# Performance work log

Hardware: AMD Instinct MI355X
Metric: run time of the kernel (lower is better)

The kernel has to match this reference:

```python
import jax, jax.numpy as jnp
import numpy as np

S = 32
D = S * S          # d = 1024 grid points
DK = 64
R = 4              # heads
NB = 3             # blocks
IN_DIM = 64
EPS = 1e-5
DX = 2.0 / (S - 1)
DXDY = DX * DX
SCALE = 1.0 / np.sqrt(float(DK))


def _edge():
    # grid[i,j] = (gx[i], gx[j]); gridT is the transpose ordering
    gx = jnp.linspace(-1.0, 1.0, S, dtype=jnp.float32)
    g = jnp.stack(jnp.meshgrid(gx, gx, indexing='ij'), axis=-1)  # [S,S,2]
    grid = g.reshape(D, 2)
    gridT = g.transpose(1, 0, 2).reshape(D, 2)
    return jnp.concatenate([
        jnp.broadcast_to(grid[:, None, :], (D, D, 2)),
        jnp.broadcast_to(gridT[None, :, :], (D, D, 2)),
    ], axis=-1)  # [D, D, 4]


def _mlp(e, W1, b1, W2, b2, W3, b3):
    # DenseNet([4,32,64,1], LeakyReLU): two hidden LeakyReLU layers, linear head
    h = jax.nn.leaky_relu(e @ W1 + b1)
    h = jax.nn.leaky_relu(h @ W2 + b2)
    return h @ W3 + b3


def _ln(v, g, b):
    # LayerNorm over normalized_shape [2d, input_dim] -> reduce last two axes
    m = jnp.mean(v, axis=(1, 2), keepdims=True)
    var = jnp.var(v, axis=(1, 2), keepdims=True)
    return (v - m) * jax.lax.rsqrt(var + EPS) * g + b


def setup_inputs() -> dict:
    key = jax.random.key(0)
    ks = jax.random.split(key, 24)
    f32 = jnp.float32

    def nrm(k, shape, fan):
        return jax.random.normal(k, shape, f32) / np.sqrt(float(fan))

    inp = {
        'x': jax.random.normal(ks[0], (8, D, 1), f32),
        'xy': jax.random.normal(ks[1], (8, 2 * D, IN_DIM), f32),
        'P': jnp.zeros((1,), f32),
        # kernel MLP (edge -> weight)
        'kW1': nrm(ks[2], (4, 32), 4), 'kb1': jnp.zeros((32,), f32),
        'kW2': nrm(ks[3], (32, 64), 32), 'kb2': jnp.zeros((64,), f32),
        'kW3': nrm(ks[4], (64, 1), 64), 'kb3': jnp.zeros((1,), f32),
        # kernelf MLP (edge -> weightf)
        'fW1': nrm(ks[5], (4, 32), 4), 'fb1': jnp.zeros((32,), f32),
        'fW2': nrm(ks[6], (32, 64), 32), 'fb2': jnp.zeros((64,), f32),
        'fW3': nrm(ks[7], (64, 1), 64), 'fb3': jnp.zeros((1,), f32),
        # per-(block, head) Q/K linear layers
        'Wq': nrm(ks[8], (NB, R, IN_DIM, DK), IN_DIM),
        'bq': jnp.zeros((NB, R, DK), f32),
        'Wk': nrm(ks[9], (NB, R, IN_DIM, DK), IN_DIM),
        'bk': jnp.zeros((NB, R, DK), f32),
        # per-block LayerNorm affine params over [2d, input_dim]
        'ln_g': jnp.ones((NB, 2 * D, IN_DIM), f32),
        'ln_b': jnp.zeros((NB, 2 * D, IN_DIM), f32),
    }
    return inp


def _forward(x, xy, P, kW1, kb1, kW2, kb2, kW3, kb3,
             fW1, fb1, fW2, fb2, fW3, fb3, Wq, bq, Wk, bk, ln_g, ln_b):
    edge = _edge()
    weight = _mlp(edge, kW1, kb1, kW2, kb2, kW3, kb3).reshape(D, D)   # shared over batch
    weightf = _mlp(edge, fW1, fb1, fW2, fb2, fW3, fb3).reshape(D, D)

    Vinput = _ln(xy, ln_g[0], ln_b[0])  # [b, 2d, in]

    for j in range(NB - 1):
        mid = jnp.zeros_like(Vinput)
        for i in range(R):
            Q = Vinput @ Wq[j, i] + bq[j, i]  # [b, 2d, dk]
            K = Vinput @ Wk[j, i] + bk[j, i]
            Attn = jnp.einsum('bnk,bmk->bnm', Q, K) * SCALE  # [b, 2d, 2d]
            mid = mid + DXDY * jnp.einsum('bnm,bmi->bni', Attn, Vinput)
        Vinput = _ln(mid, ln_g[j + 1], ln_b[j + 1]) + Vinput

    b = xy.shape[0]
    out = jnp.zeros((b, IN_DIM, D), xy.dtype)
    xy_d = xy[:, :D, :]  # [b, d, in]
    for i in range(R):
        Q = Vinput @ Wq[NB - 1, i] + bq[NB - 1, i]
        K = Vinput @ Wk[NB - 1, i] + bk[NB - 1, i]
        Au = jnp.einsum('bnk,bmk->bnm', Q[:, :D], K[:, :D]) * SCALE  # Attn[:, :d, :d]
        Af = jnp.einsum('bnk,bmk->bnm', Q[:, D:], K[:, :D]) * SCALE  # Attn[:, d:, :d]
        Vu = DXDY * jnp.einsum('bnm,bmi->bin', Au, xy_d)  # [b, in, d]
        Vf = DXDY * jnp.einsum('bnm,bmi->bin', Af, xy_d)
        out = out + DXDY * (Vu @ weight) + DXDY * (Vf @ weightf)
    return out.transpose(0, 2, 1)  # [b, d, in]


def reference(x, xy, P, kW1, kb1, kW2, kb2, kW3, kb3,
              fW1, fb1, fW2, fb2, fW3, fb3, Wq, bq, Wk, bk, ln_g, ln_b):
    return _forward(x, xy, P, kW1, kb1, kW2, kb2, kW3, kb3,
                    fW1, fb1, fW2, fb2, fW3, fb3, Wq, bq, Wk, bk, ln_g, ln_b)
```

## Files before the change

kernel.cpp:

```cpp
#include <hip/hip_runtime.h>

namespace {
constexpr int SD = 1024;
constexpr int TD = 2048;
constexpr int BATCH = 8;
constexpr int RH = 4;
constexpr float EPSc = 1e-5f;
constexpr float DXf = 2.0f / 31.0f;
constexpr float DXDYf = DXf * DXf;
constexpr float SCALEf = 0.125f;
constexpr float CFINAL = DXDYf * DXDYf * SCALEf;

constexpr size_t OFF_V   = 0;
constexpr size_t OFF_MID = OFF_V   + (size_t)BATCH * TD * 64;
constexpr size_t OFF_W   = OFF_MID + (size_t)BATCH * TD * 64;
constexpr size_t OFF_WF  = OFF_W   + (size_t)SD * SD;
constexpr size_t OFF_U1K = OFF_WF  + (size_t)SD * SD;
constexpr size_t OFF_U2K = OFF_U1K + SD * 32;
constexpr size_t OFF_U1F = OFF_U2K + SD * 32;
constexpr size_t OFF_U2F = OFF_U1F + SD * 32;
constexpr size_t OFF_GP  = OFF_U2F + SD * 32;
constexpr size_t OFF_SP  = OFF_GP  + (size_t)BATCH * 32 * 4096;
constexpr size_t OFF_A   = OFF_SP  + BATCH * 32 * 64;
constexpr size_t OFF_RV  = OFF_A   + BATCH * 4096;
constexpr size_t OFF_LNP = OFF_RV  + BATCH * 64;
constexpr size_t OFF_ZU  = OFF_LNP + BATCH * 32 * 2;
constexpr size_t OFF_ZF  = OFF_ZU  + (size_t)SD * 512;
constexpr size_t OFF_W1  = OFF_ZF  + (size_t)SD * 512;
constexpr size_t OFF_CS  = OFF_W1  + SD;
constexpr size_t WS_FLOATS = OFF_CS + 16 * SD;
constexpr size_t LIN_OFF = 50704;
}

typedef __bf16 bf16x8 __attribute__((ext_vector_type(8)));
typedef float f32x4 __attribute__((ext_vector_type(4)));

__device__ __forceinline__ float leaky(float x) { return fmaxf(x, 0.01f * x); }
__device__ __forceinline__ float gxv(int i) { return -1.0f + (2.0f / 31.0f) * (float)i; }
__device__ __forceinline__ ushort f2bf(float x) { union { __bf16 b; ushort u; } v; v.b = (__bf16)x; return v.u; }
__device__ __forceinline__ float bf2f(ushort u) { return __uint_as_float(((uint)u) << 16); }

__global__ __launch_bounds__(256) void k_prep(
    const float* __restrict__ kW1, const float* __restrict__ kb1,
    const float* __restrict__ fW1, const float* __restrict__ fb1,
    float* __restrict__ u1k, float* __restrict__ u2k,
    float* __restrict__ u1f, float* __restrict__ u2f,
    const float* __restrict__ kW2, const float* __restrict__ kW3, const float* __restrict__ kb2,
    const float* __restrict__ fW2, const float* __restrict__ fW3, const float* __restrict__ fb2,
    float* __restrict__ LIN,
    const float* __restrict__ Wq, const float* __restrict__ bq,
    const float* __restrict__ Wk, const float* __restrict__ bk,
    float* __restrict__ Ep, float* __restrict__ fp,
    float* __restrict__ gp, float* __restrict__ cp,
    const float* __restrict__ xy, float* __restrict__ part) {
  __shared__ __align__(16) float Wqs[4096];
  __shared__ float Wks[64 * 65];
  __shared__ float bqs[64], bks[64];
  __shared__ float ss4[4], qq4[4];
  int blk = blockIdx.x, t = threadIdx.x;
  if (blk >= 16) {
    int idx = blk - 16;
    int b = idx >> 5, c = idx & 31;
    const float4* X4 = reinterpret_cast<const float4*>(xy + (size_t)b * 131072 + (size_t)c * 4096);
    float s = 0.f, q = 0.f;
#pragma unroll
    for (int k = 0; k < 4; k++) {
      float4 v = X4[t + k * 256];
      s += v.x + v.y + v.z + v.w;
      q += v.x * v.x + v.y * v.y + v.z * v.z + v.w * v.w;
    }
    for (int off = 32; off; off >>= 1) { s += __shfl_down(s, off); q += __shfl_down(q, off); }
    int lane = t & 63, wid = t >> 6;
    if (lane == 0) { ss4[wid] = s; qq4[wid] = q; }
    __syncthreads();
    if (t == 0) {
      part[(size_t)(b * 32 + c) * 2] = ss4[0] + ss4[1] + ss4[2] + ss4[3];
      part[(size_t)(b * 32 + c) * 2 + 1] = qq4[0] + qq4[1] + qq4[2] + qq4[3];
    }
    return;
  }
  if (blk < 4) {
    int n = blk * 256 + t;
    float ga = gxv(n >> 5), gb = gxv(n & 31);
    for (int j = 0; j < 32; j++) {
      u1k[n * 32 + j] = ga * kW1[j] + gb * kW1[32 + j] + kb1[j];
      u2k[n * 32 + j] = gb * kW1[64 + j] + ga * kW1[96 + j];
      u1f[n * 32 + j] = ga * fW1[j] + gb * fW1[32 + j] + fb1[j];
      u2f[n * 32 + j] = gb * fW1[64 + j] + ga * fW1[96 + j];
    }
    if (blk < 2 && t < 33) {
      const float* W2 = blk ? fW2 : kW2;
      const float* W3 = blk ? fW3 : kW3;
      const float* b2 = blk ? fb2 : kb2;
      if (t < 32) {
        float s = 0.f;
        for (int o = 0; o < 64; o++) s += W2[t * 64 + o] * W3[o];
        LIN[blk * 32 + t] = s;
      } else {
        float s = 0.f;
        for (int o = 0; o < 64; o++) s += b2[o] * W3[o];
        LIN[64 + blk] = s;
      }
    }
    return;
  }
  int h = blk - 4;
  const float* wqb = Wq + (size_t)h * 4096;
  const float* wkb = Wk + (size_t)h * 4096;
  for (int idx = t; idx < 4096; idx += 256) {
    Wqs[idx] = wqb[idx];
    Wks[(idx >> 6) * 65 + (idx & 63)] = wkb[idx];
  }
  if (t < 64) { bqs[t] = bq[h * 64 + t]; bks[t] = bk[h * 64 + t]; }
  __syncthreads();
  int cpp = t & 63, cb = (t >> 6) * 16;
  float acc[16];
#pragma unroll
  for (int u = 0; u < 16; u++) acc[u] = 0.f;
  for (int k = 0; k < 64; k++) {
    float wkv = Wks[cpp * 65 + k];
#pragma unroll
    for (int u = 0; u < 16; u++) acc[u] += Wqs[(cb + u) * 64 + k] * wkv;
  }
  float* eo = Ep + (size_t)h * 4096;
#pragma unroll
  for (int u = 0; u < 16; u++) eo[(cb + u) * 64 + cpp] = acc[u];
  if (t < 64) {
    float f = 0.f, gg = 0.f;
    for (int k = 0; k < 64; k++) {
      f  += Wqs[t * 64 + k] * bks[k];
      gg += Wks[t * 65 + k] * bqs[k];
    }
    fp[h * 64 + t] = f;
    gp[h * 64 + t] = gg;
    float ca = bqs[t] * bks[t];
    ca += __shfl_xor(ca, 1, 64);
    ca += __shfl_xor(ca, 2, 64);
    ca += __shfl_xor(ca, 4, 64);
    ca += __shfl_xor(ca, 8, 64);
    ca += __shfl_xor(ca, 16, 64);
    ca += __shfl_xor(ca, 32, 64);
    if (t == 0) cp[h] = ca;
  }
}

__global__ __launch_bounds__(256) void k_mlp2apply(
    const float* __restrict__ u1k, const float* __restrict__ u2k,
    const float* __restrict__ kW2, const float* __restrict__ kb2,
    const float* __restrict__ kW3, const float* __restrict__ kb3,
    const float* __restrict__ u1f, const float* __restrict__ u2f,
    const float* __restrict__ fW2, const float* __restrict__ fb2,
    const float* __restrict__ fW3, const float* __restrict__ fb3,
    const float* __restrict__ LIN,
    ushort* __restrict__ outK, ushort* __restrict__ outF,
    const float* __restrict__ src, const float* __restrict__ g,
    const float* __restrict__ bb, const float* __restrict__ lnp,
    float* __restrict__ Vout, float* __restrict__ Gp, float* __restrict__ sp) {
  __shared__ __align__(16) float Vs[4096];
  __shared__ float sm[2];
  int blk = blockIdx.x;
  const int t = threadIdx.x;
  if (blk < 1024) {
    const int which = blk >> 9;
    const int nb = blk & 511;
    const float* u1 = which ? u1f : u1k;
    const float* u2 = which ? u2f : u2k;
    const float* W2 = which ? fW2 : kW2;
    const float* b2 = which ? fb2 : kb2;
    const float* W3 = which ? fW3 : kW3;
    const float* b3 = which ? fb3 : kb3;
    ushort* out = which ? outF : outK;
    const int lane = t & 63, wave = t >> 6;
    const int row = lane & 15, grp = lane >> 4;
    const int n0 = (nb >> 1) * 4;
    const int mh = nb & 1;

    bf16x8 wfrag[4];
    float4 b2q[4], w3q[4];
#pragma unroll
    for (int tt = 0; tt < 4; tt++) {
#pragma unroll
      for (int i = 0; i < 8; i++) wfrag[tt][i] = (__bf16)W2[(grp * 8 + i) * 64 + tt * 16 + row];
      b2q[tt] = *reinterpret_cast<const float4*>(b2 + tt * 16 + grp * 4);
      w3q[tt] = *reinterpret_cast<const float4*>(W3 + tt * 16 + grp * 4);
    }
    float4 l0 = *reinterpret_cast<const float4*>(LIN + which * 32 + grp * 8);
    float4 l1 = *reinterpret_cast<const float4*>(LIN + which * 32 + grp * 8 + 4);
    float linp[8] = {l0.x, l0.y, l0.z, l0.w, l1.x, l1.y, l1.z, l1.w};
    const float cst = 0.505f * LIN[64 + which] + b3[0];

    float u1j[4][8];
#pragma unroll
    for (int nn = 0; nn < 4; nn++)
#pragma unroll
      for (int i = 0; i < 8; i++) u1j[nn][i] = u1[(n0 + nn) * 32 + grp * 8 + i];

#pragma unroll
    for (int chunk = 0; chunk < 2; chunk++) {
#pragma unroll
      for (int st = 0; st < 4; st++) {
        int mbase = mh * 512 + chunk * 256 + wave * 64 + st * 16;
        int m = mbase + row;
        const float4* u2p = reinterpret_cast<const float4*>(u2 + (size_t)m * 32 + grp * 8);
        float4 ua = u2p[0], ub = u2p[1];
        float hv[8] = {ua.x, ua.y, ua.z, ua.w, ub.x, ub.y, ub.z, ub.w};
#pragma unroll
        for (int nn = 0; nn < 4; nn++) {
          float h1f[8];
#pragma unroll
          for (int i = 0; i < 8; i++) h1f[i] = leaky(u1j[nn][i] + hv[i]);
          float accLin = 0.f;
#pragma unroll
          for (int i = 0; i < 8; i++) accLin = fmaf(linp[i], h1f[i], accLin);
          bf16x8 pfrag;
#pragma unroll
          for (int i = 0; i < 8; i++) pfrag[i] = (__bf16)h1f[i];
          float accAbs = 0.f;
#pragma unroll
          for (int tt = 0; tt < 4; tt++) {
            f32x4 ci = {b2q[tt].x, b2q[tt].y, b2q[tt].z, b2q[tt].w};
            f32x4 c = __builtin_amdgcn_mfma_f32_16x16x32_bf16(wfrag[tt], pfrag, ci, 0, 0, 0);
            accAbs = fmaf(fabsf(c[0]), w3q[tt].x, accAbs);
            accAbs = fmaf(fabsf(c[1]), w3q[tt].y, accAbs);
            accAbs = fmaf(fabsf(c[2]), w3q[tt].z, accAbs);
            accAbs = fmaf(fabsf(c[3]), w3q[tt].w, accAbs);
          }
          float red = fmaf(0.495f, accAbs, 0.505f * accLin);
          red += __shfl_xor(red, 16, 64);
          red += __shfl_xor(red, 32, 64);
          if (grp == 0) out[(size_t)(n0 + nn) * SD + mbase + row] = f2bf(red + cst);
        }
      }
    }
    return;
  }
  int idx2 = blk - 1024;
  int c = idx2 & 31, b = idx2 >> 5;
  if (t == 0) {
    float s = 0.f, q = 0.f;
    for (int cc = 0; cc < 32; cc++) {
      s += lnp[(size_t)(b * 32 + cc) * 2];
      q += lnp[(size_t)(b * 32 + cc) * 2 + 1];
    }
    float mean = s / 131072.0f;
    sm[0] = mean;
    sm[1] = rsqrtf(q / 131072.0f - mean * mean + EPSc);
  }
  __syncthreads();
  float mean = sm[0], is = sm[1];
  size_t base4 = (size_t)b * 32768 + (size_t)c * 1024;
#pragma unroll
  for (int k = 0; k < 4; k++) {
    int idx = t + k * 256;
    float4 v = reinterpret_cast<const float4*>(src)[base4 + idx];
    float4 gg = reinterpret_cast<const float4*>(g)[c * 1024 + idx];
    float4 bv = reinterpret_cast<const float4*>(bb)[c * 1024 + idx];
    float4 r;
    r.x = (v.x - mean) * is * gg.x + bv.x;
    r.y = (v.y - mean) * is * gg.y + bv.y;
    r.z = (v.z - mean) * is * gg.z + bv.z;
    r.w = (v.w - mean) * is * gg.w + bv.w;
    reinterpret_cast<float4*>(Vout)[base4 + idx] = r;
    reinterpret_cast<float4*>(Vs)[idx] = r;
  }
  __syncthreads();
  int tp = t >> 4, tq = t & 15;
  float a2[4][4] = {};
  for (int k = 0; k < 64; k++) {
    float4 xv = *reinterpret_cast<const float4*>(&Vs[k * 64 + tp * 4]);
    float4 yv = *reinterpret_cast<const float4*>(&Vs[k * 64 + tq * 4]);
    a2[0][0] += xv.x * yv.x; a2[0][1] += xv.x * yv.y; a2[0][2] += xv.x * yv.z; a2[0][3] += xv.x * yv.w;
    a2[1][0] += xv.y * yv.x; a2[1][1] += xv.y * yv.y; a2[1][2] += xv.y * yv.z; a2[1][3] += xv.y * yv.w;
    a2[2][0] += xv.z * yv.x; a2[2][1] += xv.z * yv.y; a2[2][2] += xv.z * yv.z; a2[2][3] += xv.z * yv.w;
    a2[3][0] += xv.w * yv.x; a2[3][1] += xv.w * yv.y; a2[3][2] += xv.w * yv.z; a2[3][3] += xv.w * yv.w;
  }
  float* go = Gp + (size_t)(b * 32 + c) * 4096;
#pragma unroll
  for (int i = 0; i < 4; i++) {
    float4 w = {a2[i][0], a2[i][1], a2[i][2], a2[i][3]};
    *reinterpret_cast<float4*>(&go[(tp * 4 + i) * 64 + tq * 4]) = w;
  }
  if (t < 64) {
    float s = 0.f;
    for (int k = 0; k < 64; k++) s += Vs[k * 64 + t];
    sp[(size_t)(b * 32 + c) * 64 + t] = s;
  }
}

__global__ __launch_bounds__(256) void k_cvtgred(
    const ushort* __restrict__ srcA, const ushort* __restrict__ srcB,
    ushort* __restrict__ dstA, ushort* __restrict__ dstB,
    const float* __restrict__ Gp, const float* __restrict__ sp,
    float* __restrict__ G, float* __restrict__ sv) {
  __shared__ float T[64][65];
  int blk = blockIdx.x, t = threadIdx.x;
  if (blk < 512) {
    int bx = blk & 15, by = (blk >> 4) & 15, bz = blk >> 8;
    const ushort* srcp = bz ? srcB : srcA;
    ushort* dst = bz ? dstB : dstA;
    int c0 = bx * 64, r0 = by * 64;
    int rr = t >> 2, cc = (t & 3) * 16;
    const uint4* s4 = reinterpret_cast<const uint4*>(srcp + (size_t)(r0 + rr) * 1024 + c0 + cc);
    uint4 q0 = s4[0], q1 = s4[1];
    uint qs[8] = {q0.x, q0.y, q0.z, q0.w, q1.x, q1.y, q1.z, q1.w};
#pragma unroll
    for (int j = 0; j < 8; j++) {
      T[rr][cc + 2 * j]     = bf2f((ushort)(qs[j] & 0xffffu));
      T[rr][cc + 2 * j + 1] = bf2f((ushort)(qs[j] >> 16));
    }
    __syncthreads();
    uint pk[8];
#pragma unroll
    for (int j = 0; j < 8; j++) {
      uint lo = (uint)f2bf(T[cc + 2 * j][rr]);
      uint hi = (uint)f2bf(T[cc + 2 * j + 1][rr]);
      pk[j] = lo | (hi << 16);
    }
    ushort* dp = dst + (size_t)(c0 + rr) * 1024 + r0 + cc;
    uint4* dp4 = reinterpret_cast<uint4*>(dp);
    dp4[0] = make_uint4(pk[0], pk[1], pk[2], pk[3]);
    dp4[1] = make_uint4(pk[4], pk[5], pk[6], pk[7]);
    return;
  }
  int idx2 = blk - 512;
  int gblk = idx2 & 15, b = idx2 >> 4;
  int idx = gblk * 256 + t;
  float a = 0.f;
  for (int c = 0; c < 32; c++) a += Gp[(size_t)(b * 32 + c) * 4096 + idx];
  G[(size_t)b * 4096 + idx] = a;
  if (gblk == 0 && t < 64) {
    float s = 0.f;
    for (int c = 0; c < 32; c++) s += sp[(size_t)(b * 32 + c) * 64 + t];
    sv[b * 64 + t] = s;
  }
}

__global__ __launch_bounds__(256) void k_gred(const float* __restrict__ Gp, const float* __restrict__ sp,
                                              float* __restrict__ G, float* __restrict__ sv, int nch) {
  int blk = blockIdx.x, b = blockIdx.y, t = threadIdx.x;
  int idx = blk * 256 + t;
  float a = 0.f;
  for (int c = 0; c < nch; c++) a += Gp[(size_t)(b * nch + c) * 4096 + idx];
  G[(size_t)b * 4096 + idx] = a;
  if (blk == 0 && t < 64) {
    float s = 0.f;
    for (int c = 0; c < nch; c++) s += sp[(size_t)(b * nch + c) * 64 + t];
    sv[b * 64 + t] = s;
  }
}

__global__ __launch_bounds__(256) void k_headsA2(
    const float* __restrict__ G, const float* __restrict__ sv,
    const float* __restrict__ Ep, const float* __restrict__ fp,
    const float* __restrict__ gp, const float* __restrict__ cp,
    int j, float scale, int doStats,
    float* __restrict__ A, float* __restrict__ RVo, float* __restrict__ STAT) {
  int b = blockIdx.x, t = threadIdx.x;
  __shared__ float Es[64 * 65];
  __shared__ __align__(16) float Gs[4096];
  __shared__ __align__(16) float As[4096];
  __shared__ float ss[64], fs[64], gs[64];
  __shared__ float cj;
  __shared__ float redbuf[8];
  const float* e0 = Ep + (size_t)(j * RH) * 4096;
  for (int idx = t; idx < 4096; idx += 256) {
    float e = e0[idx] + e0[idx + 4096] + e0[idx + 8192] + e0[idx + 12288];
    Es[(idx >> 6) * 65 + (idx & 63)] = e;
    Gs[idx] = G[(size_t)b * 4096 + idx];
  }
  if (t < 64) {
    ss[t] = sv[b * 64 + t];
    int h0 = j * RH * 64;
    fs[t] = fp[h0 + t] + fp[h0 + 64 + t] + fp[h0 + 128 + t] + fp[h0 + 192 + t];
    gs[t] = gp[h0 + t] + gp[h0 + 64 + t] + gp[h0 + 128 + t] + gp[h0 + 192 + t];
  }
  if (t == 0) cj = cp[j * RH] + cp[j * RH + 1] + cp[j * RH + 2] + cp[j * RH + 3];
  __syncthreads();
  int c = t >> 2, qb = (t & 3) * 16;
  float fv = fs[c];
  float4 acc[4];
#pragma unroll
  for (int u = 0; u < 4; u++) {
    acc[u].x = fv * ss[qb + u * 4 + 0];
    acc[u].y = fv * ss[qb + u * 4 + 1];
    acc[u].z = fv * ss[qb + u * 4 + 2];
    acc[u].w = fv * ss[qb + u * 4 + 3];
  }
  for (int d = 0; d < 64; d++) {
    float ev = Es[c * 65 + d];
    const float4* gr = reinterpret_cast<const float4*>(&Gs[d * 64 + qb]);
#pragma unroll
    for (int u = 0; u < 4; u++) {
      float4 gv = gr[u];
      acc[u].x += ev * gv.x; acc[u].y += ev * gv.y; acc[u].z += ev * gv.z; acc[u].w += ev * gv.w;
    }
  }
  float* ao = A + (size_t)b * 4096 + c * 64 + qb;
#pragma unroll
  for (int u = 0; u < 4; u++) {
    float4 v = acc[u];
    v.x *= scale; v.y *= scale; v.z *= scale; v.w *= scale;
    reinterpret_cast<float4*>(ao)[u] = v;
    *reinterpret_cast<float4*>(&As[c * 64 + qb + u * 4]) = v;
  }
  float rv_t = 0.f;
  if (t < 64) {
    float r = cj * ss[t];
    for (int d = 0; d < 64; d++) r += gs[d] * Gs[d * 64 + t];
    r *= scale;
    RVo[b * 64 + t] = r;
    rv_t = r;
  }
  if (!doStats) return;
  __syncthreads();
  float4 h[4] = {};
  for (int d = 0; d < 64; d++) {
    float gvv = Gs[c * 64 + d];
    const float4* ar = reinterpret_cast<const float4*>(&As[d * 64 + qb]);
#pragma unroll
    for (int u = 0; u < 4; u++) {
      float4 av = ar[u];
      h[u].x += gvv * av.x; h[u].y += gvv * av.y; h[u].z += gvv * av.z; h[u].w += gvv * av.w;
    }
  }
  float tp_ = 0.f;
#pragma unroll
  for (int u = 0; u < 4; u++) {
    float4 a = *reinterpret_cast<const float4*>(&As[c * 64 + qb + u * 4]);
    tp_ += a.x * h[u].x + a.y * h[u].y + a.z * h[u].z + a.w * h[u].w;
  }
  tp_ += __shfl_xor(tp_, 1, 64);  tp_ += __shfl_xor(tp_, 2, 64);
  tp_ += __shfl_xor(tp_, 4, 64);  tp_ += __shfl_xor(tp_, 8, 64);
  tp_ += __shfl_xor(tp_, 16, 64); tp_ += __shfl_xor(tp_, 32, 64);
  if ((t & 63) == 0) redbuf[t >> 6] = tp_;
  if (t < 64) {
    float t1 = 0.f;
    for (int d = 0; d < 64; d++) t1 += ss[d] * As[d * 64 + t];
    float s1 = t1, sr = rv_t, sr2 = rv_t * rv_t, srt = rv_t * t1;
#pragma unroll
    for (int off = 1; off < 64; off <<= 1) {
      s1  += __shfl_xor(s1, off, 64);
      sr  += __shfl_xor(sr, off, 64);
      sr2 += __shfl_xor(sr2, off, 64);
      srt += __shfl_xor(srt, off, 64);
    }
    if (t == 0) { redbuf[4] = s1; redbuf[5] = sr; redbuf[6] = sr2; redbuf[7] = srt; }
  }
  __syncthreads();
  if (t == 0) {
    float tr = redbuf[0] + redbuf[1] + redbuf[2] + redbuf[3];
    float smid = redbuf[4] + 2048.0f * redbuf[5];
    float mu = smid / 131072.0f;
    float e2 = (tr + 2.0f * redbuf[7] + 2048.0f * redbuf[6]) / 131072.0f;
    STAT[b * 2] = mu;
    STAT[b * 2 + 1] = rsqrtf(e2 - mu * mu + EPSc);
  }
}

__global__ __launch_bounds__(256) void k_midapply(
    float* __restrict__ V, const float* __restrict__ A,
    const float* __restrict__ RVv, const float* __restrict__ STAT,
    const float* __restrict__ g, const float* __restrict__ bb,
    const float* __restrict__ Yext,
    float* __restrict__ Gp, float* __restrict__ sp, int nchG) {
  int blk = blockIdx.x, b = blockIdx.y, t = threadIdx.x;
  __shared__ __align__(16) float As[4096];
  __shared__ __align__(16) float Vs[4096];
  __shared__ __align__(16) float Ys[4096];
  __shared__ float rs[64];
  __shared__ float sm[2];
  const float4* A4 = reinterpret_cast<const float4*>(A + (size_t)b * 4096);
#pragma unroll
  for (int k = 0; k < 4; k++) reinterpret_cast<float4*>(As)[t + k * 256] = A4[t + k * 256];
  if (t < 64) rs[t] = RVv[b * 64 + t];
  if (t == 0) { sm[0] = STAT[b * 2]; sm[1] = STAT[b * 2 + 1]; }
  bool doG = (blk < nchG);
  if (Yext != nullptr && doG) {
    size_t yb = (size_t)b * 32768 + (size_t)blk * 1024;
#pragma unroll
    for (int k = 0; k < 4; k++)
      reinterpret_cast<float4*>(Ys)[t + k * 256] = reinterpret_cast<const float4*>(Yext)[yb + t + k * 256];
  }
  __syncthreads();
  float mu = sm[0], is = sm[1];
  int rl = t >> 2, qb = (t & 3) * 16;
  int row = blk * 64 + rl;
  float* vr = V + (size_t)b * 131072 + (size_t)row * 64;
  float4 acc[4];
#pragma unroll
  for (int u = 0; u < 4; u++) {
    acc[u].x = rs[qb + u * 4 + 0]; acc[u].y = rs[qb + u * 4 + 1];
    acc[u].z = rs[qb + u * 4 + 2]; acc[u].w = rs[qb + u * 4 + 3];
  }
  for (int c = 0; c < 64; c++) {
    float vv = vr[c];
    const float4* ar = reinterpret_cast<const float4*>(&As[c * 64 + qb]);
#pragma unroll
    for (int u = 0; u < 4; u++) {
      float4 av = ar[u];
      acc[u].x += vv * av.x; acc[u].y += vv * av.y; acc[u].z += vv * av.z; acc[u].w += vv * av.w;
    }
  }
  const float4* g4 = reinterpret_cast<const float4*>(g + (size_t)row * 64 + qb);
  const float4* b4 = reinterpret_cast<const float4*>(bb + (size_t)row * 64 + qb);
  const float4* vq = reinterpret_cast<const float4*>(vr + qb);
  float4* vo = reinterpret_cast<float4*>(vr + qb);
#pragma unroll
  for (int u = 0; u < 4; u++) {
    float4 gg = g4[u], bv = b4[u], av = vq[u];
    float4 r;
    r.x = (acc[u].x - mu) * is * gg.x + bv.x + av.x;
    r.y = (acc[u].y - mu) * is * gg.y + bv.y + av.y;
    r.z = (acc[u].z - mu) * is * gg.z + bv.z + av.z;
    r.w = (acc[u].w - mu) * is * gg.w + bv.w + av.w;
    vo[u] = r;
    *reinterpret_cast<float4*>(&Vs[rl * 64 + qb + u * 4]) = r;
  }
  __syncthreads();
  if (!doG) return;
  const float* Yp = (Yext != nullptr) ? Ys : Vs;
  int tp = t >> 4, tq = t & 15;
  float a2[4][4] = {};
  for (int k = 0; k < 64; k++) {
    float4 xv = *reinterpret_cast<const float4*>(&Vs[k * 64 + tp * 4]);
    float4 yv = *reinterpret_cast<const float4*>(&Yp[k * 64 + tq * 4]);
    a2[0][0] += xv.x * yv.x; a2[0][1] += xv.x * yv.y; a2[0][2] += xv.x * yv.z; a2[0][3] += xv.x * yv.w;
    a2[1][0] += xv.y * yv.x; a2[1][1] += xv.y * yv.y; a2[1][2] += xv.y * yv.z; a2[1][3] += xv.y * yv.w;
    a2[2][0] += xv.z * yv.x; a2[2][1] += xv.z * yv.y; a2[2][2] += xv.z * yv.z; a2[2][3] += xv.z * yv.w;
    a2[3][0] += xv.w * yv.x; a2[3][1] += xv.w * yv.y; a2[3][2] += xv.w * yv.z; a2[3][3] += xv.w * yv.w;
  }
  float* go = Gp + (size_t)(b * nchG + blk) * 4096;
#pragma unroll
  for (int i = 0; i < 4; i++) {
    float4 w = {a2[i][0], a2[i][1], a2[i][2], a2[i][3]};
    *reinterpret_cast<float4*>(&go[(tp * 4 + i) * 64 + tq * 4]) = w;
  }
  if (t < 64) {
    float s = 0.f;
    for (int k = 0; k < 64; k++) s += Yp[k * 64 + t];
    sp[(size_t)(b * nchG + blk) * 64 + t] = s;
  }
}

__global__ __launch_bounds__(256) void k_y(const float* __restrict__ V, const float* __restrict__ A,
                                           ushort* __restrict__ ZT) {
  int blk = blockIdx.x, b = blockIdx.y, z = blockIdx.z, t = threadIdx.x;
  __shared__ __align__(16) float As[4096];
  __shared__ ushort Zs[64][36];
  const float4* A4 = reinterpret_cast<const float4*>(A + (size_t)b * 4096);
#pragma unroll
  for (int k = 0; k < 4; k++) reinterpret_cast<float4*>(As)[t + k * 256] = A4[t + k * 256];
  __syncthreads();
  int ml = t >> 3, qb = (t & 7) * 8;
  int m = blk * 32 + ml;
  const float* vr = V + (size_t)b * 131072 + (size_t)(z * 1024 + m) * 64;
  float4 acc[2] = {};
  for (int c = 0; c < 64; c++) {
    float vv = vr[c];
    const float4* ar = reinterpret_cast<const float4*>(&As[c * 64 + qb]);
#pragma unroll
    for (int u = 0; u < 2; u++) {
      float4 av = ar[u];
      acc[u].x += vv * av.x; acc[u].y += vv * av.y; acc[u].z += vv * av.z; acc[u].w += vv * av.w;
    }
  }
  Zs[qb + 0][ml] = f2bf(acc[0].x); Zs[qb + 1][ml] = f2bf(acc[0].y);
  Zs[qb + 2][ml] = f2bf(acc[0].z); Zs[qb + 3][ml] = f2bf(acc[0].w);
  Zs[qb + 4][ml] = f2bf(acc[1].x); Zs[qb + 5][ml] = f2bf(acc[1].y);
  Zs[qb + 6][ml] = f2bf(acc[1].z); Zs[qb + 7][ml] = f2bf(acc[1].w);
  __syncthreads();
  int rowq = t >> 2, seg = t & 3;
  const ushort* srcp = &Zs[rowq][seg * 8];
  uint p0 = (uint)srcp[0] | ((uint)srcp[1] << 16);
  uint p1 = (uint)srcp[2] | ((uint)srcp[3] << 16);
  uint p2 = (uint)srcp[4] | ((uint)srcp[5] << 16);
  uint p3 = (uint)srcp[6] | ((uint)srcp[7] << 16);
  ushort* dp = ZT + (size_t)(b * 64 + rowq) * 2048 + (size_t)z * 1024 + blk * 32 + seg * 8;
  *reinterpret_cast<uint4*>(dp) = make_uint4(p0, p1, p2, p3);
}

__global__ __launch_bounds__(256) void k_final_mfma2(const ushort* __restrict__ WTW,
                                                     const ushort* __restrict__ WTF,
                                                     const ushort* __restrict__ ZT,
                                                     const float* __restrict__ RV,
                                                     float* __restrict__ out) {
  int tn = blockIdx.x, tb = blockIdx.y, t = threadIdx.x;
  int lane = t & 63, w = t >> 6;
  int wn = w & 1, wb = w >> 1;
  int r = lane & 15, g = lane >> 4;
  int nrow = tn * 32 + wn * 16 + r;
  int bi0 = tb * 64 + wb * 32 + r;
  bf16x8 ones;
#pragma unroll
  for (int i = 0; i < 8; i++) ones[i] = (__bf16)1.0f;
  f32x4 a0 = {0.f, 0.f, 0.f, 0.f}, a1 = a0, aw = a0;
  for (int kz = 0; kz < 4; kz++) {
    const ushort* wbase = (kz < 2) ? WTW : WTF;
    const ushort* wp = wbase + (size_t)nrow * 1024 + (kz & 1) * 512 + g * 8;
    const ushort* zp0 = ZT + (size_t)bi0 * 2048 + kz * 512 + g * 8;
    const ushort* zp1 = zp0 + 16 * 2048;
#pragma unroll 4
    for (int ks = 0; ks < 512; ks += 32) {
      bf16x8 fa  = *reinterpret_cast<const bf16x8*>(wp + ks);
      bf16x8 fb0 = *reinterpret_cast<const bf16x8*>(zp0 + ks);
      bf16x8 fb1 = *reinterpret_cast<const bf16x8*>(zp1 + ks);
      a0 = __builtin_amdgcn_mfma_f32_16x16x32_bf16(fa, fb0, a0, 0, 0, 0);
      a1 = __builtin_amdgcn_mfma_f32_16x16x32_bf16(fa, fb1, a1, 0, 0, 0);
      aw = __builtin_amdgcn_mfma_f32_16x16x32_bf16(fa, ones, aw, 0, 0, 0);
    }
  }
  int nbase = tn * 32 + wn * 16 + g * 4;
  int i0 = wb * 32 + r;
  float rv0 = RV[tb * 64 + i0];
  float rv1 = RV[tb * 64 + i0 + 16];
  float* op = out + (size_t)tb * 65536;
#pragma unroll
  for (int rr = 0; rr < 4; rr++) {
    float w1v = aw[rr];
    op[(size_t)(nbase + rr) * 64 + i0]      = CFINAL * (a0[rr] + w1v * rv0);
    op[(size_t)(nbase + rr) * 64 + i0 + 16] = CFINAL * (a1[rr] + w1v * rv1);
  }
}

extern "C" void kernel_launch(void* const* d_in, const int* in_sizes, int n_in,
                              void* d_out, int out_size, void* d_ws, size_t ws_size,
                              hipStream_t stream) {
  (void)in_sizes; (void)n_in; (void)out_size;
  const float* xy  = (const float*)d_in[1];
  const float* kW1 = (const float*)d_in[3];
  const float* kb1 = (const float*)d_in[4];
  const float* kW2 = (const float*)d_in[5];
  const float* kb2 = (const float*)d_in[6];
  const float* kW3 = (const float*)d_in[7];
  const float* kb3 = (const float*)d_in[8];
  const float* fW1 = (const float*)d_in[9];
  const float* fb1 = (const float*)d_in[10];
  const float* fW2 = (const float*)d_in[11];
  const float* fb2 = (const float*)d_in[12];
  const float* fW3 = (const float*)d_in[13];
  const float* fb3 = (const float*)d_in[14];
  const float* Wq  = (const float*)d_in[15];
  const float* bq  = (const float*)d_in[16];
  const float* Wk  = (const float*)d_in[17];
  const float* bk  = (const float*)d_in[18];
  const float* lng = (const float*)d_in[19];
  const float* lnb = (const float*)d_in[20];
  float* ws = (float*)d_ws;
  float* out = (float*)d_out;
  if (ws_size < WS_FLOATS * sizeof(float)) return;

  float* V   = ws + OFF_V;
  float* U1K = ws + OFF_U1K;
  float* U2K = ws + OFF_U2K;
  float* U1F = ws + OFF_U1F;
  float* U2F = ws + OFF_U2F;
  float* GPb = ws + OFF_GP;
  float* SPb = ws + OFF_SP;
  float* LNP = ws + OFF_LNP;
  float* G    = ws + OFF_U1K;
  float* SV   = ws + OFF_U1F;
  float* A    = ws + OFF_A;
  float* RV   = ws + OFF_RV;
  float* STAT = ws + OFF_LNP;
  ushort* Wbf  = (ushort*)(ws + OFF_W);
  ushort* WTW  = (ushort*)(ws + OFF_W + 524288);
  ushort* Wfbf = (ushort*)(ws + OFF_WF);
  ushort* WTF  = (ushort*)(ws + OFF_WF + 524288);
  ushort* ZT   = (ushort*)(ws + OFF_MID);
  float* Ep   = ws + OFF_ZU;
  float* Fp   = ws + OFF_ZU + 49152;
  float* Gpp  = ws + OFF_ZU + 49920;
  float* Cp   = ws + OFF_ZU + 50688;
  float* LIN  = ws + OFF_ZU + LIN_OFF;

  k_prep<<<dim3(272), dim3(256), 0, stream>>>(kW1, kb1, fW1, fb1, U1K, U2K, U1F, U2F,
                                              kW2, kW3, kb2, fW2, fW3, fb2, LIN,
                                              Wq, bq, Wk, bk, Ep, Fp, Gpp, Cp,
                                              xy, LNP);
  k_mlp2apply<<<dim3(1280), dim3(256), 0, stream>>>(U1K, U2K, kW2, kb2, kW3, kb3,
                                                    U1F, U2F, fW2, fb2, fW3, fb3, LIN, Wbf, Wfbf,
                                                    xy, lng, lnb, LNP, V, GPb, SPb);
  k_cvtgred<<<dim3(640), dim3(256), 0, stream>>>(Wbf, Wfbf, WTW, WTF, GPb, SPb, G, SV);

  for (int j = 0; j < 2; j++) {
    k_headsA2<<<dim3(8), dim3(256), 0, stream>>>(G, SV, Ep, Fp, Gpp, Cp, j, DXDYf * SCALEf, 1,
                                                 A, RV, STAT);
    k_midapply<<<dim3(32, 8), dim3(256), 0, stream>>>(
        V, A, RV, STAT, lng + (size_t)(j + 1) * 131072, lnb + (size_t)(j + 1) * 131072,
        (j == 1) ? xy : nullptr, GPb, SPb, (j == 1) ? 16 : 32);
    k_gred<<<dim3(16, 8), dim3(256), 0, stream>>>(GPb, SPb, G, SV, (j == 1) ? 16 : 32);
  }
  k_headsA2<<<dim3(8), dim3(256), 0, stream>>>(G, SV, Ep, Fp, Gpp, Cp, 2, 1.0f, 0, A, RV, STAT);
  k_y<<<dim3(32, 8, 2), dim3(256), 0, stream>>>(V, A, ZT);
  k_final_mfma2<<<dim3(32, 8), dim3(256), 0, stream>>>(WTW, WTF, ZT, RV, out);
}
```

Before: 160.3 us.

## Pre-sum per-head projection products in prep and halve final MFMA tile

The prep kernel now accumulates the four heads' Wq·Wk^T, bias and constant terms inside one block per layer, so the heads kernel reads one summed matrix instead of adding four per head. The final MFMA kernel drops its second accumulator: each wave computes a single 16x16 tile and the grid doubles to 64x8 blocks, giving more parallelism. In exchange, prep runs heads serially with extra syncs in fewer blocks, and the W operand loads are no longer shared across two batch tiles.

```diff
diff --git a/kernel.cpp b/kernel.cpp
--- a/kernel.cpp
+++ b/kernel.cpp
@@ -50,8 +50,8 @@
     float* __restrict__ LIN,
     const float* __restrict__ Wq, const float* __restrict__ bq,
     const float* __restrict__ Wk, const float* __restrict__ bk,
-    float* __restrict__ Ep, float* __restrict__ fp,
-    float* __restrict__ gp, float* __restrict__ cp,
+    float* __restrict__ Ej, float* __restrict__ fj,
+    float* __restrict__ gj, float* __restrict__ cj,
     const float* __restrict__ xy, float* __restrict__ part) {
   __shared__ __align__(16) float Wqs[4096];
   __shared__ float Wks[64 * 65];
@@ -104,43 +104,51 @@
     }
     return;
   }
-  int h = blk - 4;
-  const float* wqb = Wq + (size_t)h * 4096;
-  const float* wkb = Wk + (size_t)h * 4096;
-  for (int idx = t; idx < 4096; idx += 256) {
-    Wqs[idx] = wqb[idx];
-    Wks[(idx >> 6) * 65 + (idx & 63)] = wkb[idx];
-  }
-  if (t < 64) { bqs[t] = bq[h * 64 + t]; bks[t] = bk[h * 64 + t]; }
-  __syncthreads();
+  int j = blk - 4;
+  if (j >= 3) return;
   int cpp = t & 63, cb = (t >> 6) * 16;
   float acc[16];
 #pragma unroll
   for (int u = 0; u < 16; u++) acc[u] = 0.f;
-  for (int k = 0; k < 64; k++) {
-    float wkv = Wks[cpp * 65 + k];
-#pragma unroll
-    for (int u = 0; u < 16; u++) acc[u] += Wqs[(cb + u) * 64 + k] * wkv;
-  }
-  float* eo = Ep + (size_t)h * 4096;
+  float facc = 0.f, gacc = 0.f, cacc = 0.f;
+  for (int i = 0; i < RH; i++) {
+    int h = j * RH + i;
+    __syncthreads();
+    const float* wqb = Wq + (size_t)h * 4096;
+    const float* wkb = Wk + (size_t)h * 4096;
+    for (int idx = t; idx < 4096; idx += 256) {
+      Wqs[idx] = wqb[idx];
+      Wks[(idx >> 6) * 65 + (idx & 63)] = wkb[idx];
+    }
+    if (t < 64) { bqs[t] = bq[h * 64 + t]; bks[t] = bk[h * 64 + t]; }
+    __syncthreads();
+    for (int k = 0; k < 64; k++) {
+      float wkv = Wks[cpp * 65 + k];
+#pragma unroll
+      for (int u = 0; u < 16; u++) acc[u] += Wqs[(cb + u) * 64 + k] * wkv;
+    }
+    if (t < 64) {
+      for (int k = 0; k < 64; k++) {
+        facc += Wqs[t * 64 + k] * bks[k];
+        gacc += Wks[t * 65 + k] * bqs[k];
+      }
+      cacc += bqs[t] * bks[t];
+    }
+  }
+  float* eo = Ej + (size_t)j * 4096;
 #pragma unroll
   for (int u = 0; u < 16; u++) eo[(cb + u) * 64 + cpp] = acc[u];
   if (t < 64) {
-    float f = 0.f, gg = 0.f;
-    for (int k = 0; k < 64; k++) {
-      f  += Wqs[t * 64 + k] * bks[k];
-      gg += Wks[t * 65 + k] * bqs[k];
-    }
-    fp[h * 64 + t] = f;
-    gp[h * 64 + t] = gg;
-    float ca = bqs[t] * bks[t];
+    fj[j * 64 + t] = facc;
+    gj[j * 64 + t] = gacc;
+    float ca = cacc;
     ca += __shfl_xor(ca, 1, 64);
     ca += __shfl_xor(ca, 2, 64);
     ca += __shfl_xor(ca, 4, 64);
     ca += __shfl_xor(ca, 8, 64);
     ca += __shfl_xor(ca, 16, 64);
     ca += __shfl_xor(ca, 32, 64);
-    if (t == 0) cp[h] = ca;
+    if (t == 0) cj[j] = ca;
   }
 }
 
@@ -351,8 +359,8 @@
 
 __global__ __launch_bounds__(256) void k_headsA2(
     const float* __restrict__ G, const float* __restrict__ sv,
-    const float* __restrict__ Ep, const float* __restrict__ fp,
-    const float* __restrict__ gp, const float* __restrict__ cp,
+    const float* __restrict__ Ej, const float* __restrict__ fj,
+    const float* __restrict__ gj, const float* __restrict__ cjp,
     int j, float scale, int doStats,
     float* __restrict__ A, float* __restrict__ RVo, float* __restrict__ STAT) {
   int b = blockIdx.x, t = threadIdx.x;
@@ -362,19 +370,17 @@
   __shared__ float ss[64], fs[64], gs[64];
   __shared__ float cj;
   __shared__ float redbuf[8];
-  const float* e0 = Ep + (size_t)(j * RH) * 4096;
+  const float* e0 = Ej + (size_t)j * 4096;
   for (int idx = t; idx < 4096; idx += 256) {
-    float e = e0[idx] + e0[idx + 4096] + e0[idx + 8192] + e0[idx + 12288];
-    Es[(idx >> 6) * 65 + (idx & 63)] = e;
+    Es[(idx >> 6) * 65 + (idx & 63)] = e0[idx];
     Gs[idx] = G[(size_t)b * 4096 + idx];
   }
   if (t < 64) {
     ss[t] = sv[b * 64 + t];
-    int h0 = j * RH * 64;
-    fs[t] = fp[h0 + t] + fp[h0 + 64 + t] + fp[h0 + 128 + t] + fp[h0 + 192 + t];
-    gs[t] = gp[h0 + t] + gp[h0 + 64 + t] + gp[h0 + 128 + t] + gp[h0 + 192 + t];
-  }
-  if (t == 0) cj = cp[j * RH] + cp[j * RH + 1] + cp[j * RH + 2] + cp[j * RH + 3];
+    fs[t] = fj[j * 64 + t];
+    gs[t] = gj[j * 64 + t];
+  }
+  if (t == 0) cj = cjp[j];
   __syncthreads();
   int c = t >> 2, qb = (t & 3) * 16;
   float fv = fs[c];
@@ -586,39 +592,32 @@
                                                      float* __restrict__ out) {
   int tn = blockIdx.x, tb = blockIdx.y, t = threadIdx.x;
   int lane = t & 63, w = t >> 6;
-  int wn = w & 1, wb = w >> 1;
   int r = lane & 15, g = lane >> 4;
-  int nrow = tn * 32 + wn * 16 + r;
-  int bi0 = tb * 64 + wb * 32 + r;
+  int nrow = tn * 16 + r;
+  int bi0 = tb * 64 + w * 16 + r;
   bf16x8 ones;
 #pragma unroll
   for (int i = 0; i < 8; i++) ones[i] = (__bf16)1.0f;
-  f32x4 a0 = {0.f, 0.f, 0.f, 0.f}, a1 = a0, aw = a0;
+  f32x4 a0 = {0.f, 0.f, 0.f, 0.f}, aw = a0;
   for (int kz = 0; kz < 4; kz++) {
     const ushort* wbase = (kz < 2) ? WTW : WTF;
     const ushort* wp = wbase + (size_t)nrow * 1024 + (kz & 1) * 512 + g * 8;
     const ushort* zp0 = ZT + (size_t)bi0 * 2048 + kz * 512 + g * 8;
-    const ushort* zp1 = zp0 + 16 * 2048;
 #pragma unroll 4
     for (int ks = 0; ks < 512; ks += 32) {
       bf16x8 fa  = *reinterpret_cast<const bf16x8*>(wp + ks);
       bf16x8 fb0 = *reinterpret_cast<const bf16x8*>(zp0 + ks);
-      bf16x8 fb1 = *reinterpret_cast<const bf16x8*>(zp1 + ks);
       a0 = __builtin_amdgcn_mfma_f32_16x16x32_bf16(fa, fb0, a0, 0, 0, 0);
-      a1 = __builtin_amdgcn_mfma_f32_16x16x32_bf16(fa, fb1, a1, 0, 0, 0);
       aw = __builtin_amdgcn_mfma_f32_16x16x32_bf16(fa, ones, aw, 0, 0, 0);
     }
   }
-  int nbase = tn * 32 + wn * 16 + g * 4;
-  int i0 = wb * 32 + r;
+  int nbase = tn * 16 + g * 4;
+  int i0 = w * 16 + r;
   float rv0 = RV[tb * 64 + i0];
-  float rv1 = RV[tb * 64 + i0 + 16];
   float* op = out + (size_t)tb * 65536;
 #pragma unroll
   for (int rr = 0; rr < 4; rr++) {
-    float w1v = aw[rr];
-    op[(size_t)(nbase + rr) * 64 + i0]      = CFINAL * (a0[rr] + w1v * rv0);
-    op[(size_t)(nbase + rr) * 64 + i0 + 16] = CFINAL * (a1[rr] + w1v * rv1);
+    op[(size_t)(nbase + rr) * 64 + i0] = CFINAL * (a0[rr] + aw[rr] * rv0);
   }
 }
 
@@ -667,15 +666,15 @@
   ushort* Wfbf = (ushort*)(ws + OFF_WF);
   ushort* WTF  = (ushort*)(ws + OFF_WF + 524288);
   ushort* ZT   = (ushort*)(ws + OFF_MID);
-  float* Ep   = ws + OFF_ZU;
-  float* Fp   = ws + OFF_ZU + 49152;
-  float* Gpp  = ws + OFF_ZU + 49920;
-  float* Cp   = ws + OFF_ZU + 50688;
+  float* Ej   = ws + OFF_ZU;
+  float* Fj   = ws + OFF_ZU + 49152;
+  float* Gj   = ws + OFF_ZU + 49920;
+  float* Cj   = ws + OFF_ZU + 50688;
   float* LIN  = ws + OFF_ZU + LIN_OFF;
 
   k_prep<<<dim3(272), dim3(256), 0, stream>>>(kW1, kb1, fW1, fb1, U1K, U2K, U1F, U2F,
                                               kW2, kW3, kb2, fW2, fW3, fb2, LIN,
-                                              Wq, bq, Wk, bk, Ep, Fp, Gpp, Cp,
+                                              Wq, bq, Wk, bk, Ej, Fj, Gj, Cj,
                                               xy, LNP);
   k_mlp2apply<<<dim3(1280), dim3(256), 0, stream>>>(U1K, U2K, kW2, kb2, kW3, kb3,
                                                     U1F, U2F, fW2, fb2, fW3, fb3, LIN, Wbf, Wfbf,
@@ -683,14 +682,14 @@
   k_cvtgred<<<dim3(640), dim3(256), 0, stream>>>(Wbf, Wfbf, WTW, WTF, GPb, SPb, G, SV);
 
   for (int j = 0; j < 2; j++) {
-    k_headsA2<<<dim3(8), dim3(256), 0, stream>>>(G, SV, Ep, Fp, Gpp, Cp, j, DXDYf * SCALEf, 1,
+    k_headsA2<<<dim3(8), dim3(256), 0, stream>>>(G, SV, Ej, Fj, Gj, Cj, j, DXDYf * SCALEf, 1,
                                                  A, RV, STAT);
     k_midapply<<<dim3(32, 8), dim3(256), 0, stream>>>(
         V, A, RV, STAT, lng + (size_t)(j + 1) * 131072, lnb + (size_t)(j + 1) * 131072,
         (j == 1) ? xy : nullptr, GPb, SPb, (j == 1) ? 16 : 32);
     k_gred<<<dim3(16, 8), dim3(256), 0, stream>>>(GPb, SPb, G, SV, (j == 1) ? 16 : 32);
   }
-  k_headsA2<<<dim3(8), dim3(256), 0, stream>>>(G, SV, Ep, Fp, Gpp, Cp, 2, 1.0f, 0, A, RV, STAT);
+  k_headsA2<<<dim3(8), dim3(256), 0, stream>>>(G, SV, Ej, Fj, Gj, Cj, 2, 1.0f, 0, A, RV, STAT);
   k_y<<<dim3(32, 8, 2), dim3(256), 0, stream>>>(V, A, ZT);
-  k_final_mfma2<<<dim3(32, 8), dim3(256), 0, stream>>>(WTW, WTF, ZT, RV, out);
-}
+  k_final_mfma2<<<dim3(64, 8), dim3(256), 0, stream>>>(WTW, WTF, ZT, RV, out);
+}
```

Measured after the change: 190.6 us. 1.19x slower.
